# Kernel optimization log

Measured on AMD Instinct MI355X. Metric: run time of the kernel, lower is better.

## Reference

```python
import jax, jax.numpy as jnp
import numpy as np

NUM_LAYERS = 4
UNITS = 512
DX = 8e-6
WAVELENGTHS = np.array([4.5e-7, 5.32e-7, 6.33e-7], dtype=np.float32)
Z_LAYERS = 0.03
Z_PROP = 0.05
NUM_MODES = 16
BASE_IDX = 1  # base_wavelength_idx in source


def setup_inputs() -> dict:
    key = jax.random.key(0)
    k1, k2 = jax.random.split(key)
    C = len(WAVELENGTHS)
    x = jax.random.normal(k1, (NUM_MODES, C, UNITS, UNITS), dtype=jnp.float32)
    # phase = rand(units, units) * pi, one per layer
    phases = jax.random.uniform(k2, (NUM_LAYERS, UNITS, UNITS), dtype=jnp.float32) * np.pi
    # wavelength_coefficients initialized to base_wavelength / wl (learned params)
    base = WAVELENGTHS[BASE_IDX]
    coeffs = jnp.tile(jnp.asarray(base / WAVELENGTHS, dtype=jnp.float32), (NUM_LAYERS, 1))
    lams = jnp.asarray(WAVELENGTHS)
    return {"x": x, "phases": phases, "coeffs": coeffs, "lams": lams}


def _transfer_fn(lams, z, n, dx):
    # Band-limited angular-spectrum transfer function, per wavelength: [C, H, W]
    f = jnp.fft.fftfreq(n, d=dx).astype(jnp.float32)
    fx2 = f[None, :] ** 2 + f[:, None] ** 2          # [H, W]
    arg = (1.0 / lams)[:, None, None] ** 2 - fx2[None]  # [C, H, W]
    valid = arg > 0
    kz = 2.0 * jnp.pi * jnp.sqrt(jnp.where(valid, arg, 0.0))
    return jnp.where(valid, jnp.exp(1j * (kz * z).astype(jnp.float32)), 0.0)


def _propagate(field, Hf):
    # field: [B, C, H, W] complex; Hf: [C, H, W] — batched angular-spectrum step
    return jnp.fft.ifft2(jnp.fft.fft2(field) * Hf[None])


def reference(x, phases, coeffs, lams):
    n = x.shape[-1]
    H_layer = _transfer_fn(lams, Z_LAYERS, n, DX)  # inter-layer propagation
    H_final = _transfer_fn(lams, Z_PROP, n, DX)    # propagation to detector
    field = x.astype(jnp.complex64)
    for l in range(NUM_LAYERS):
        # per-wavelength effective phase: phase * coeff (depth_factor == 1)
        eff = phases[l][None, :, :] * coeffs[l][:, None, None]  # [C, H, W]
        field = field * jnp.exp(1j * eff)[None]
        field = _propagate(field, H_layer)
    field = _propagate(field, H_final)
    return jnp.abs(field) ** 2
```

## Files before the change

kernel.cpp:

```cpp
#include <hip/hip_runtime.h>
#include <hip/hip_fp16.h>
#include <math.h>


#define TWOPI_F 6.2831854820251465f
#define RSQ2    0.70710678f
#define NPIX    (48*512*512)

__device__ __forceinline__ float2 cadd(float2 a, float2 b){ return make_float2(a.x+b.x, a.y+b.y); }
__device__ __forceinline__ float2 csub(float2 a, float2 b){ return make_float2(a.x-b.x, a.y-b.y); }
__device__ __forceinline__ float2 cmul(float2 a, float2 b){ return make_float2(a.x*b.x - a.y*b.y, a.x*b.y + a.y*b.x); }

template<int S> __device__ __forceinline__ float2 mul_i(float2 a){
  return (S>0) ? make_float2(-a.y, a.x) : make_float2(a.y, -a.x);
}
template<int S> __device__ __forceinline__ float2 mul_w1(float2 a){
  return (S>0) ? make_float2(RSQ2*(a.x-a.y), RSQ2*(a.x+a.y))
               : make_float2(RSQ2*(a.x+a.y), RSQ2*(a.y-a.x));
}
template<int S> __device__ __forceinline__ float2 mul_w3(float2 a){
  return (S>0) ? make_float2(RSQ2*(-a.x-a.y), RSQ2*(a.x-a.y))
               : make_float2(RSQ2*(a.y-a.x), RSQ2*(-a.x-a.y));
}
template<int S> __device__ __forceinline__ float2 cmul_tw(float2 v, float2 w){
  float wy = (S>0) ? -w.y : w.y;
  return make_float2(v.x*w.x - v.y*wy, v.x*wy + v.y*w.x);
}

__device__ __forceinline__ float4 f4add(float4 a, float4 b){ return make_float4(a.x+b.x,a.y+b.y,a.z+b.z,a.w+b.w); }
__device__ __forceinline__ float4 f4sub(float4 a, float4 b){ return make_float4(a.x-b.x,a.y-b.y,a.z-b.z,a.w-b.w); }
template<int S> __device__ __forceinline__ float4 mul_i4(float4 a){
  return (S>0) ? make_float4(-a.y,a.x,-a.w,a.z) : make_float4(a.y,-a.x,a.w,-a.z);
}
template<int S> __device__ __forceinline__ float4 mul_w14(float4 a){
  return (S>0) ? make_float4(RSQ2*(a.x-a.y), RSQ2*(a.x+a.y), RSQ2*(a.z-a.w), RSQ2*(a.z+a.w))
               : make_float4(RSQ2*(a.x+a.y), RSQ2*(a.y-a.x), RSQ2*(a.z+a.w), RSQ2*(a.w-a.z));
}
template<int S> __device__ __forceinline__ float4 mul_w34(float4 a){
  return (S>0) ? make_float4(RSQ2*(-a.x-a.y), RSQ2*(a.x-a.y), RSQ2*(-a.z-a.w), RSQ2*(a.z-a.w))
               : make_float4(RSQ2*(a.y-a.x), RSQ2*(-a.x-a.y), RSQ2*(a.w-a.z), RSQ2*(-a.z-a.w));
}
template<int S> __device__ __forceinline__ float4 cmul_tw4(float4 v, float2 w){
  float wy = (S>0) ? -w.y : w.y;
  return make_float4(v.x*w.x - v.y*wy, v.x*wy + v.y*w.x,
                     v.z*w.x - v.w*wy, v.z*wy + v.w*w.x);
}
__device__ __forceinline__ float4 cmulh4(float4 v, float4 h){
  return make_float4(v.x*h.x - v.y*h.y, v.x*h.y + v.y*h.x,
                     v.z*h.z - v.w*h.w, v.z*h.w + v.w*h.z);
}

template<int S>
__device__ __forceinline__ void dft8(const float2* a, float2* d){
  float2 b0=cadd(a[0],a[4]), b1=cadd(a[1],a[5]), b2=cadd(a[2],a[6]), b3=cadd(a[3],a[7]);
  float2 b4=csub(a[0],a[4]);
  float2 b5=mul_w1<S>(csub(a[1],a[5]));
  float2 b6=mul_i<S> (csub(a[2],a[6]));
  float2 b7=mul_w3<S>(csub(a[3],a[7]));
  float2 c0=cadd(b0,b2), c2=csub(b0,b2);
  float2 c1=cadd(b1,b3), c3=mul_i<S>(csub(b1,b3));
  float2 c4=cadd(b4,b6), c6=csub(b4,b6);
  float2 c5=cadd(b5,b7), c7=mul_i<S>(csub(b5,b7));
  d[0]=cadd(c0,c1); d[1]=csub(c0,c1);
  d[2]=cadd(c2,c3); d[3]=csub(c2,c3);
  d[4]=cadd(c4,c5); d[5]=csub(c4,c5);
  d[6]=cadd(c6,c7); d[7]=csub(c6,c7);
}
template<int S>
__device__ __forceinline__ void dft8_4(const float4* a, float4* d){
  float4 b0=f4add(a[0],a[4]), b1=f4add(a[1],a[5]), b2=f4add(a[2],a[6]), b3=f4add(a[3],a[7]);
  float4 b4=f4sub(a[0],a[4]);
  float4 b5=mul_w14<S>(f4sub(a[1],a[5]));
  float4 b6=mul_i4<S> (f4sub(a[2],a[6]));
  float4 b7=mul_w34<S>(f4sub(a[3],a[7]));
  float4 c0=f4add(b0,b2), c2=f4sub(b0,b2);
  float4 c1=f4add(b1,b3), c3=mul_i4<S>(f4sub(b1,b3));
  float4 c4=f4add(b4,b6), c6=f4sub(b4,b6);
  float4 c5=f4add(b5,b7), c7=mul_i4<S>(f4sub(b5,b7));
  d[0]=f4add(c0,c1); d[1]=f4sub(c0,c1);
  d[2]=f4add(c2,c3); d[3]=f4sub(c2,c3);
  d[4]=f4add(c4,c5); d[5]=f4sub(c4,c5);
  d[6]=f4add(c6,c7); d[7]=f4sub(c6,c7);
}

__device__ __forceinline__ int SWZR(int i){ return i ^ ((i>>4)&7); }
__device__ __forceinline__ int CSWZ(int e, int cx){ return (e<<3) + (cx ^ ((e>>3)&7)); }

__device__ __forceinline__ void lds_fence(){ asm volatile("s_waitcnt lgkmcnt(0)" ::: "memory"); }

__device__ __forceinline__ void make_tw(int t, float2* tw0, float2* tw1){
  float sn, cs;
  __sincosf((TWOPI_F/512.0f)*(float)t, &sn, &cs);
  float2 w0 = make_float2(cs, -sn);
  tw0[0] = make_float2(1.0f, 0.0f);
  #pragma unroll
  for(int k=1;k<8;k++) tw0[k] = cmul(tw0[k-1], w0);
  int p = t>>3;
  __sincosf((TWOPI_F/64.0f)*(float)p, &sn, &cs);
  float2 w1 = make_float2(cs, -sn);
  tw1[0] = make_float2(1.0f, 0.0f);
  #pragma unroll
  for(int k=1;k<8;k++) tw1[k] = cmul(tw1[k-1], w1);
}

template<int S>
__device__ __forceinline__ void fft512_wv(float2* a, float2* o, float2* B, int t,
                                          float scale, const float2* tw0, const float2* tw1){
  const int km[8] = {0,4,2,6,1,5,3,7};
  float2 d[8];
  dft8<S>(a, d);
  #pragma unroll
  for(int k=0;k<8;k++)
    B[SWZR(8*t+k)] = (k==0) ? d[0] : cmul_tw<S>(d[km[k]], tw0[k]);
  lds_fence();
  #pragma unroll
  for(int r=0;r<8;r++) a[r] = B[SWZR(t+64*r)];
  lds_fence();
  dft8<S>(a, d);
  {
    int p = t>>3, q = t&7;
    #pragma unroll
    for(int k=0;k<8;k++)
      B[SWZR(q + 64*p + 8*k)] = (k==0) ? d[0] : cmul_tw<S>(d[km[k]], tw1[k]);
  }
  lds_fence();
  #pragma unroll
  for(int r=0;r<8;r++) a[r] = B[SWZR(t+64*r)];
  lds_fence();
  dft8<S>(a, d);
  #pragma unroll
  for(int k=0;k<8;k++) o[k] = make_float2(d[km[k]].x*scale, d[km[k]].y*scale);
}

template<int S>
__device__ __forceinline__ void fft512_pr(float4* a, float4* o, float4* B, int t, int cx,
                                          float scale, const float2* tw0, const float2* tw1){
  const int km[8] = {0,4,2,6,1,5,3,7};
  float4 d[8];
  dft8_4<S>(a, d);
  #pragma unroll
  for(int k=0;k<8;k++)
    B[CSWZ(8*t+k, cx)] = (k==0) ? d[0] : cmul_tw4<S>(d[km[k]], tw0[k]);
  __syncthreads();
  #pragma unroll
  for(int r=0;r<8;r++) a[r] = B[CSWZ(t+64*r, cx)];
  __syncthreads();
  dft8_4<S>(a, d);
  {
    int p = t>>3, q = t&7;
    #pragma unroll
    for(int k=0;k<8;k++)
      B[CSWZ(q + 64*p + 8*k, cx)] = (k==0) ? d[0] : cmul_tw4<S>(d[km[k]], tw1[k]);
  }
  __syncthreads();
  #pragma unroll
  for(int r=0;r<8;r++) a[r] = B[CSWZ(t+64*r, cx)];
  dft8_4<S>(a, d);
  #pragma unroll
  for(int k=0;k<8;k++)
    o[k] = make_float4(d[km[k]].x*scale, d[km[k]].y*scale, d[km[k]].z*scale, d[km[k]].w*scale);
}

template<int S, int LD>
__device__ __forceinline__ void fft512_1b(float2* a, float2* o, float2* B, int t,
                                          float scale, const float2* tw0, const float2* tw1){
  const int km[8] = {0,4,2,6,1,5,3,7};
  float2 d[8];
  dft8<S>(a, d);
  #pragma unroll
  for(int k=0;k<8;k++)
    B[(8*t+k)*LD] = (k==0) ? d[0] : cmul_tw<S>(d[km[k]], tw0[k]);
  __syncthreads();
  #pragma unroll
  for(int r=0;r<8;r++) a[r] = B[(t+64*r)*LD];
  __syncthreads();
  dft8<S>(a, d);
  {
    int p = t>>3, q = t&7;
    #pragma unroll
    for(int k=0;k<8;k++)
      B[(q + 64*p + 8*k)*LD] = (k==0) ? d[0] : cmul_tw<S>(d[km[k]], tw1[k]);
  }
  __syncthreads();
  #pragma unroll
  for(int r=0;r<8;r++) a[r] = B[(t+64*r)*LD];
  dft8<S>(a, d);
  #pragma unroll
  for(int k=0;k<8;k++) o[k] = make_float2(d[km[k]].x*scale, d[km[k]].y*scale);
}


struct AccH {
  __half2* p;
  __device__ __forceinline__ float2 ld(int i) const { return __half22float2(p[i]); }
  __device__ __forceinline__ void   st(int i, float2 v) const { p[i] = __floats2half2_rn(v.x, v.y); }
};
struct AccS {
  float* re; float* im;
  __device__ __forceinline__ float2 ld(int i) const { return make_float2(re[i], im[i]); }
  __device__ __forceinline__ void   st(int i, float2 v) const { re[i]=v.x; im[i]=v.y; }
};


__device__ __forceinline__ float2 phase_of(float kz, float zf){
  float tt = __fmul_rn(kz, zf);
  double dt = (double)tt;
  double q  = rint(dt * 0.15915494309189535);
  double rr = fma(-q, 6.283185307179586, dt);
  float sn, cs; __sincosf((float)rr, &sn, &cs);
  return make_float2(cs, sn);
}

__global__ __launch_bounds__(256) void k_htab(const float* __restrict__ lams,
                                              float2* __restrict__ H1, float2* __restrict__ H12){
  int e = blockIdx.x*256 + threadIdx.x;
  int c = e >> 18, fy = (e>>9)&511, col = e&511;
  const float lam = lams[c];
  const float il  = 1.0f / lam;
  const float il2 = __fmul_rn(il, il);
  const float DEN = (float)(512.0 * 8e-6);
  int   sx  = (col < 256) ? col : col - 512;
  int   sy  = (fy  < 256) ? fy  : fy  - 512;
  float fxv = (float)sx / DEN, fyv = (float)sy / DEN;
  float arg = __fsub_rn(il2, __fadd_rn(__fmul_rn(fxv,fxv), __fmul_rn(fyv,fyv)));
  float2 h1 = make_float2(0.0f,0.0f), h12 = h1;
  if(arg > 0.0f){
    float s  = (float)sqrt((double)arg);
    float kz = __fmul_rn(6.2831854820251465f, s);
    h1  = phase_of(kz, 0.03f);
    h12 = cmul(h1, phase_of(kz, 0.05f));
  }
  H1[e] = h1; H12[e] = h12;
}


template<class Acc>
__global__ __launch_bounds__(256) void k_row_first(
    const float* __restrict__ x, Acc f,
    const float* __restrict__ phases, const float* __restrict__ coeffs)
{
  __shared__ float2 lds[4][512];
  const int w = threadIdx.x >> 6, t = threadIdx.x & 63;
  const int img = blockIdx.x, c = img % 3;
  const int row = (blockIdx.y<<2) + w;
  const int base = (img*512 + row)*512;
  const float* ph = phases + row*512;
  const float coeff = coeffs[c];
  float2 tw0[8], tw1[8]; make_tw(t, tw0, tw1);
  float2 a[8], o[8];
  #pragma unroll
  for(int r=0;r<8;r++){
    int i = t + (r<<6);
    float xv = x[base+i];
    float th = __fmul_rn(ph[i], coeff);
    float sn, cs; __sincosf(th, &sn, &cs);
    a[r] = make_float2(xv*cs, xv*sn);
  }
  fft512_wv<-1>(a, o, lds[w], t, 1.0f, tw0, tw1);
  #pragma unroll
  for(int k=0;k<8;k++){ int i=t+(k<<6); f.st(base+i, o[k]); }
}

template<class Acc>
__global__ __launch_bounds__(256) void k_row_mid(
    Acc f, const float* __restrict__ phases, const float* __restrict__ coeffs, int layer)
{
  __shared__ float2 lds[4][512];
  const int w = threadIdx.x >> 6, t = threadIdx.x & 63;
  const int img = blockIdx.x, c = img % 3;
  const int row = (blockIdx.y<<2) + w;
  const int base = (img*512 + row)*512;
  const float* ph = phases + (layer*512 + row)*512;
  const float coeff = coeffs[layer*3 + c];
  float2 tw0[8], tw1[8]; make_tw(t, tw0, tw1);
  float2 a[8], o[8], pv[8];
  #pragma unroll
  for(int r=0;r<8;r++){
    int i=t+(r<<6); a[r]=f.ld(base+i);
    float th = __fmul_rn(ph[i], coeff);
    float sn, cs; __sincosf(th, &sn, &cs);
    pv[r] = make_float2(cs, sn);
  }
  fft512_wv<+1>(a, o, lds[w], t, 1.0f/512.0f, tw0, tw1);
  #pragma unroll
  for(int k=0;k<8;k++) a[k] = cmul(o[k], pv[k]);
  fft512_wv<-1>(a, o, lds[w], t, 1.0f, tw0, tw1);
  #pragma unroll
  for(int k=0;k<8;k++){ int i=t+(k<<6); f.st(base+i, o[k]); }
}

template<class Acc>
__global__ __launch_bounds__(256) void k_row_last(
    Acc f, float* __restrict__ out)
{
  __shared__ float2 lds[4][512];
  const int w = threadIdx.x >> 6, t = threadIdx.x & 63;
  const int img = blockIdx.x;
  const int row = (blockIdx.y<<2) + w;
  const int base = (img*512 + row)*512;
  float2 tw0[8], tw1[8]; make_tw(t, tw0, tw1);
  float2 a[8], o[8];
  #pragma unroll
  for(int r=0;r<8;r++){ int i=t+(r<<6); a[r]=f.ld(base+i); }
  fft512_wv<+1>(a, o, lds[w], t, 1.0f/512.0f, tw0, tw1);
  #pragma unroll
  for(int k=0;k<8;k++){ int i=t+(k<<6); out[base+i] = o[k].x*o[k].x + o[k].y*o[k].y; }
}


__global__ __launch_bounds__(512, 4) void k_colp(
    __half2* __restrict__ F, const float2* __restrict__ Htab, float2* __restrict__ Hdummy)
{
  __shared__ float4 lds[512*8];
  const int cx = threadIdx.x & 7, t = threadIdx.x >> 3;
  const int img = blockIdx.x, c = img % 3;
  const int col = (blockIdx.y<<4) + (cx<<1);
  const int ibase = (img<<18) + col;
  float2 tw0[8], tw1[8]; make_tw(t, tw0, tw1);
  float4 a[8], o[8], h[8];
  #pragma unroll
  for(int r=0;r<8;r++){
    int gi = ibase + ((t+(r<<6))<<9);
    uint2 raw = *reinterpret_cast<const uint2*>(F + gi);
    __half2 v0, v1;
    *reinterpret_cast<unsigned int*>(&v0) = raw.x;
    *reinterpret_cast<unsigned int*>(&v1) = raw.y;
    float2 fA = __half22float2(v0), fB = __half22float2(v1);
    a[r] = make_float4(fA.x, fA.y, fB.x, fB.y);
  }
  #pragma unroll
  for(int k=0;k<8;k++){
    int fy = t + (k<<6);
    h[k] = *reinterpret_cast<const float4*>(Htab + (c<<18) + (fy<<9) + col);
  }
  fft512_pr<-1>(a, o, lds, t, cx, 1.0f, tw0, tw1);
  #pragma unroll
  for(int k=0;k<8;k++) a[k] = cmulh4(o[k], h[k]);
  __syncthreads();
  fft512_pr<+1>(a, o, lds, t, cx, 1.0f/512.0f, tw0, tw1);
  #pragma unroll
  for(int k=0;k<8;k++){
    int gi = ibase + ((t+(k<<6))<<9);
    __half2 v0 = __floats2half2_rn(o[k].x, o[k].y);
    __half2 v1 = __floats2half2_rn(o[k].z, o[k].w);
    uint2 raw;
    raw.x = *reinterpret_cast<unsigned int*>(&v0);
    raw.y = *reinterpret_cast<unsigned int*>(&v1);
    *reinterpret_cast<uint2*>(F + gi) = raw;
  }
}


template<class Acc, bool TAB>
__global__ __launch_bounds__(512, 4) void k_col8(
    Acc f, const float2* __restrict__ Htab, const float* __restrict__ lams, float z1, float z2)
{
  __shared__ float2 lds[512][9];
  const int cx = threadIdx.x & 7, t = threadIdx.x >> 3;
  const int img = blockIdx.x, c = img % 3;
  const int col = (blockIdx.y<<3) + cx;
  const int ibase = (img<<18) + col;
  float2 tw0[8], tw1[8]; make_tw(t, tw0, tw1);
  float2 a[8], o[8], h[8];
  #pragma unroll
  for(int r=0;r<8;r++){ int gi = ibase + ((t+(r<<6))<<9); a[r]=f.ld(gi); }
  if(TAB){
    const float2* Hrow = Htab + (c<<18) + col;
    #pragma unroll
    for(int k=0;k<8;k++) h[k] = Hrow[(t+(k<<6))<<9];
  } else {
    const float lam = lams[c];
    const float il  = 1.0f / lam;
    const float il2 = __fmul_rn(il, il);
    const float DEN = (float)(512.0 * 8e-6);
    int   sx  = (col < 256) ? col : col - 512;
    float fxv = (float)sx / DEN;
    float fx2 = __fmul_rn(fxv, fxv);
    #pragma unroll
    for(int k=0;k<8;k++){
      int fy = t + (k<<6);
      int sy = (fy < 256) ? fy : fy - 512;
      float fyv = (float)sy / DEN;
      float arg = __fsub_rn(il2, __fadd_rn(fx2, __fmul_rn(fyv,fyv)));
      h[k] = make_float2(0.0f, 0.0f);
      if(arg > 0.0f){
        float s  = (float)sqrt((double)arg);
        float kz = __fmul_rn(6.2831854820251465f, s);
        h[k] = phase_of(kz, z1);
        if(z2 != 0.0f) h[k] = cmul(h[k], phase_of(kz, z2));
      }
    }
  }
  fft512_1b<-1,9>(a, o, &lds[0][cx], t, 1.0f, tw0, tw1);
  #pragma unroll
  for(int k=0;k<8;k++) a[k] = cmul(o[k], h[k]);
  __syncthreads();
  fft512_1b<+1,9>(a, o, &lds[0][cx], t, 1.0f/512.0f, tw0, tw1);
  #pragma unroll
  for(int k=0;k<8;k++){ int gi = ibase + ((t+(k<<6))<<9); f.st(gi, o[k]); }
}


extern "C" void kernel_launch(void* const* d_in, const int* in_sizes, int n_in,
                              void* d_out, int out_size, void* d_ws, size_t ws_size,
                              hipStream_t stream)
{
  const float* x      = (const float*)d_in[0];
  const float* phases = (const float*)d_in[1];
  const float* coeffs = (const float*)d_in[2];
  const float* lams   = (const float*)d_in[3];
  float* out = (float*)d_out;

  const size_t fldH = (size_t)NPIX*4;
  const size_t splB = (size_t)NPIX*4;
  const size_t tabB = (size_t)3*512*512*8;

  dim3 gA(48,128), bA(256);
  dim3 gP(48,32),  bP(512);
  dim3 gB(48,64),  bB(512);
  dim3 gH(3*512*512/256), bH(256);

  if(ws_size >= fldH + 2*tabB){
    AccH f { (__half2*)d_ws };
    float2* H1  = (float2*)((char*)d_ws + fldH);
    float2* H12 = H1 + 3*512*512;
    k_htab<<<gH, bH, 0, stream>>>(lams, H1, H12);
    k_row_first<AccH><<<gA, bA, 0, stream>>>(x, f, phases, coeffs);
    for(int l=1; l<=3; l++){
      k_colp<<<gP, bP, 0, stream>>>((__half2*)d_ws, H1, nullptr);
      k_row_mid<AccH><<<gA, bA, 0, stream>>>(f, phases, coeffs, l);
    }
    k_colp<<<gP, bP, 0, stream>>>((__half2*)d_ws, H12, nullptr);
    k_row_last<AccH><<<gA, bA, 0, stream>>>(f, out);
  } else if(ws_size >= splB + 2*tabB){
    AccS f { out, (float*)d_ws };
    float2* H1  = (float2*)((char*)d_ws + splB);
    float2* H12 = H1 + 3*512*512;
    k_htab<<<gH, bH, 0, stream>>>(lams, H1, H12);
    k_row_first<AccS><<<gA, bA, 0, stream>>>(x, f, phases, coeffs);
    for(int l=1; l<=3; l++){
      k_col8<AccS,true><<<gB, bB, 0, stream>>>(f, H1, lams, 0.03f, 0.0f);
      k_row_mid<AccS><<<gA, bA, 0, stream>>>(f, phases, coeffs, l);
    }
    k_col8<AccS,true><<<gB, bB, 0, stream>>>(f, H12, lams, 0.03f, 0.0f);
    k_row_last<AccS><<<gA, bA, 0, stream>>>(f, out);
  } else {
    AccS f { out, (float*)d_ws };
    k_row_first<AccS><<<gA, bA, 0, stream>>>(x, f, phases, coeffs);
    for(int l=1; l<=3; l++){
      k_col8<AccS,false><<<gB, bB, 0, stream>>>(f, nullptr, lams, 0.03f, 0.0f);
      k_row_mid<AccS><<<gA, bA, 0, stream>>>(f, phases, coeffs, l);
    }
    k_col8<AccS,false><<<gB, bB, 0, stream>>>(f, nullptr, lams, 0.03f, 0.05f);
    k_row_last<AccS><<<gA, bA, 0, stream>>>(f, out);
  }
}
```

Measured before the change: 324.4 us.

## Process two column groups per block and stage output through swizzled LDS

The column-FFT kernel now handles 32 columns per block in two sequential passes, holding the fp16 results in registers. It then writes them through a swizzled shared-memory tile so each row segment is stored with 16-byte vectorized, more contiguous global writes. The grid shrinks to half as many blocks and is reordered so column groups vary fastest. The aim is better store coalescing and less per-block setup, at the cost of more registers, a larger 64 KB LDS footprint and extra barriers, which may reduce occupancy.

```diff
diff --git a/kernel.cpp b/kernel.cpp
--- a/kernel.cpp
+++ b/kernel.cpp
@@ -308,45 +308,80 @@
 }
 
 
-__global__ __launch_bounds__(512, 4) void k_colp(
-    __half2* __restrict__ F, const float2* __restrict__ Htab, float2* __restrict__ Hdummy)
-{
-  __shared__ float4 lds[512*8];
+__global__ __launch_bounds__(512, 4) void k_colq(
+    __half2* __restrict__ F, const float2* __restrict__ Htab)
+{
+  __shared__ __align__(16) unsigned char ldsraw[65536];
+  float4*       stage = reinterpret_cast<float4*>(ldsraw);
+  unsigned int* tile  = reinterpret_cast<unsigned int*>(ldsraw);
+
   const int cx = threadIdx.x & 7, t = threadIdx.x >> 3;
-  const int img = blockIdx.x, c = img % 3;
-  const int col = (blockIdx.y<<4) + (cx<<1);
-  const int ibase = (img<<18) + col;
+  const int cg  = blockIdx.x;
+  const int img = blockIdx.y, c = img % 3;
+  const int col0 = cg << 5;
   float2 tw0[8], tw1[8]; make_tw(t, tw0, tw1);
-  float4 a[8], o[8], h[8];
-  #pragma unroll
-  for(int r=0;r<8;r++){
-    int gi = ibase + ((t+(r<<6))<<9);
-    uint2 raw = *reinterpret_cast<const uint2*>(F + gi);
-    __half2 v0, v1;
-    *reinterpret_cast<unsigned int*>(&v0) = raw.x;
-    *reinterpret_cast<unsigned int*>(&v1) = raw.y;
-    float2 fA = __half22float2(v0), fB = __half22float2(v1);
-    a[r] = make_float4(fA.x, fA.y, fB.x, fB.y);
-  }
-  #pragma unroll
-  for(int k=0;k<8;k++){
-    int fy = t + (k<<6);
-    h[k] = *reinterpret_cast<const float4*>(Htab + (c<<18) + (fy<<9) + col);
-  }
-  fft512_pr<-1>(a, o, lds, t, cx, 1.0f, tw0, tw1);
-  #pragma unroll
-  for(int k=0;k<8;k++) a[k] = cmulh4(o[k], h[k]);
-  __syncthreads();
-  fft512_pr<+1>(a, o, lds, t, cx, 1.0f/512.0f, tw0, tw1);
-  #pragma unroll
-  for(int k=0;k<8;k++){
-    int gi = ibase + ((t+(k<<6))<<9);
-    __half2 v0 = __floats2half2_rn(o[k].x, o[k].y);
-    __half2 v1 = __floats2half2_rn(o[k].z, o[k].w);
-    uint2 raw;
-    raw.x = *reinterpret_cast<unsigned int*>(&v0);
-    raw.y = *reinterpret_cast<unsigned int*>(&v1);
-    *reinterpret_cast<uint2*>(F + gi) = raw;
+  uint2 r0[8], r1[8];
+
+  #pragma unroll
+  for(int b=0; b<2; b++){
+    const int col = col0 + (b<<4) + (cx<<1);
+    const int ibase = (img<<18) + col;
+    float4 a[8], o[8], h[8];
+    #pragma unroll
+    for(int r=0;r<8;r++){
+      int gi = ibase + ((t+(r<<6))<<9);
+      uint2 raw = *reinterpret_cast<const uint2*>(F + gi);
+      __half2 v0, v1;
+      *reinterpret_cast<unsigned int*>(&v0) = raw.x;
+      *reinterpret_cast<unsigned int*>(&v1) = raw.y;
+      float2 fA = __half22float2(v0), fB = __half22float2(v1);
+      a[r] = make_float4(fA.x, fA.y, fB.x, fB.y);
+    }
+    #pragma unroll
+    for(int k=0;k<8;k++){
+      int fy = t + (k<<6);
+      h[k] = *reinterpret_cast<const float4*>(Htab + (c<<18) + (fy<<9) + col);
+    }
+    if(b) __syncthreads();
+    fft512_pr<-1>(a, o, stage, t, cx, 1.0f, tw0, tw1);
+    #pragma unroll
+    for(int k=0;k<8;k++) a[k] = cmulh4(o[k], h[k]);
+    __syncthreads();
+    fft512_pr<+1>(a, o, stage, t, cx, 1.0f/512.0f, tw0, tw1);
+    #pragma unroll
+    for(int k=0;k<8;k++){
+      __half2 v0 = __floats2half2_rn(o[k].x, o[k].y);
+      __half2 v1 = __floats2half2_rn(o[k].z, o[k].w);
+      uint2 pk;
+      pk.x = *reinterpret_cast<unsigned int*>(&v0);
+      pk.y = *reinterpret_cast<unsigned int*>(&v1);
+      if(b==0) r0[k] = pk; else r1[k] = pk;
+    }
+  }
+  __syncthreads();
+  {
+    const int s = (t&7)<<2;
+    #pragma unroll
+    for(int k=0;k<8;k++){
+      int row = t + (k<<6);
+      int cc0 = cx<<1;
+      int pc0 = (cc0 + s) & 31;
+      int pc1 = (cc0 + 16 + s) & 31;
+      *reinterpret_cast<uint2*>(tile + row*32 + pc0) = r0[k];
+      *reinterpret_cast<uint2*>(tile + row*32 + pc1) = r1[k];
+    }
+  }
+  __syncthreads();
+  {
+    const int rg = threadIdx.x >> 3, j0 = threadIdx.x & 7;
+    const int s2 = (rg&7)<<2;
+    #pragma unroll
+    for(int g=0; g<8; g++){
+      int row = rg + (g<<6);
+      int pd = ((j0<<2) + s2) & 31;
+      uint4 v = *reinterpret_cast<const uint4*>(tile + row*32 + pd);
+      *reinterpret_cast<uint4*>(F + (img<<18) + (row<<9) + col0 + (j0<<2)) = v;
+    }
   }
 }
 
@@ -416,7 +451,7 @@
   const size_t tabB = (size_t)3*512*512*8;
 
   dim3 gA(48,128), bA(256);
-  dim3 gP(48,32),  bP(512);
+  dim3 gQ(16,48),  bQ(512);
   dim3 gB(48,64),  bB(512);
   dim3 gH(3*512*512/256), bH(256);
 
@@ -427,10 +462,10 @@
     k_htab<<<gH, bH, 0, stream>>>(lams, H1, H12);
     k_row_first<AccH><<<gA, bA, 0, stream>>>(x, f, phases, coeffs);
     for(int l=1; l<=3; l++){
-      k_colp<<<gP, bP, 0, stream>>>((__half2*)d_ws, H1, nullptr);
+      k_colq<<<gQ, bQ, 0, stream>>>((__half2*)d_ws, H1);
       k_row_mid<AccH><<<gA, bA, 0, stream>>>(f, phases, coeffs, l);
     }
-    k_colp<<<gP, bP, 0, stream>>>((__half2*)d_ws, H12, nullptr);
+    k_colq<<<gQ, bQ, 0, stream>>>((__half2*)d_ws, H12);
     k_row_last<AccH><<<gA, bA, 0, stream>>>(f, out);
   } else if(ws_size >= splB + 2*tabB){
     AccS f { out, (float*)d_ws };
```

Result: slower. 386.0 us (+19.0%).
